# Optimization experiments

Hardware: AMD Instinct MI355X
Metric: run time of the kernel (lower is better)

## Reference

```python
import jax, jax.numpy as jnp
import numpy as np

N = 4096        # nodes
E = 65536       # edges (avg degree 16)
L = 64          # latent_dims
K = 256         # kernel_dims
ED = 6          # edge_dims
DEPTH = 2


def _gelu(x):
    # torch.nn.GELU / F.gelu default = exact erf form
    return jax.nn.gelu(x, approximate=False)


def setup_inputs() -> dict:
    key = jax.random.key(0)
    ks = jax.random.split(key, 12)
    u = lambda k, shape, fan: jax.random.uniform(k, shape, jnp.float32, -1.0, 1.0) / np.sqrt(fan)
    return {
        "nodes": jax.random.normal(ks[0], (N, L), jnp.float32),
        "edge_index": jax.random.randint(ks[1], (2, E), 0, N, jnp.int32),
        "edge_attr": jax.random.uniform(ks[2], (E, ED), jnp.float32),
        # DenseNet kernel MLP: ED -> K -> K -> L*L (GELU between layers)
        "W1": u(ks[3], (ED, K), ED), "b1": jnp.zeros((K,), jnp.float32),
        "W2": u(ks[4], (K, K), K),  "b2": jnp.zeros((K,), jnp.float32),
        "W3": u(ks[5], (K, L * L), K), "b3": jnp.zeros((L * L,), jnp.float32),
        # NNConv root linear (no bias) + conv bias
        "W_root": u(ks[6], (L, L), L),
        "bias": jnp.zeros((L,), jnp.float32),
    }


def reference(nodes, edge_index, edge_attr, W1, b1, W2, b2, W3, b3, W_root, bias):
    src, dst = edge_index[0], edge_index[1]
    # Edge-conditioned dynamic weights (depend only on edge_attr -> compute once)
    h = _gelu(edge_attr @ W1 + b1)          # [E, K]
    h = _gelu(h @ W2 + b2)                  # [E, K]
    W_edge = (h @ W3 + b3).reshape(E, L, L) # [E, L_in, L_out]

    def conv(x):
        msg = jnp.einsum('ei,eio->eo', x[src], W_edge)          # gather + per-edge matmul
        agg = jax.ops.segment_sum(msg, dst, num_segments=N)     # scatter-add to dst
        return agg + x @ W_root + bias

    x = nodes
    for idx in range(DEPTH):
        x = conv(x)
        if idx < DEPTH - 1:
            x = _gelu(x)
    return x
```

## Files before the change

### kernel.cpp

```cpp
#include <hip/hip_runtime.h>
#include <math.h>

#define NN 4096
#define NE 65536
#define LL 64
#define KK 256
#define ED 6
#define MAXSUPER 6144

typedef __bf16 bf16_t;
typedef __attribute__((ext_vector_type(4))) __bf16 bf16x4;
typedef __attribute__((ext_vector_type(8))) __bf16 bf16x8;
typedef __attribute__((ext_vector_type(4))) float f32x4;
typedef __attribute__((ext_vector_type(16))) float f32x16;

#define OFF_CNT    ((size_t)0)
#define OFF_DESC   ((size_t)16384)
#define OFF_AGG0   ((size_t)147456)
#define OFF_AGG1   ((size_t)1196032)
#define ZERO_BYTES ((size_t)2244608)
#define OFF_CURSOR ((size_t)2244608)
#define OFF_SORTED ((size_t)2260992)
#define OFF_W2R    ((size_t)2785280)
#define OFF_W3RR   ((size_t)2916352)
#define OFF_Q0     ((size_t)5013504)
#define OFF_Q1     ((size_t)6062080)
#define OFF_X1F    ((size_t)7110656)
#define OFF_X0BF   ((size_t)8159232)
#define OFF_X1BF   ((size_t)8683520)
#define OFF_H      ((size_t)9207808)
#define OFF_P      ((size_t)42762240)

__device__ __forceinline__ float gelu_f(float x) {
    return 0.5f * x * (1.0f + erff(x * 0.7071067811865476f));
}
__device__ __forceinline__ bf16_t f2bf(float x) { return (bf16_t)x; }

__global__ void k_hist(const int* __restrict__ ei, int* __restrict__ cnt) {
    int e = blockIdx.x * 256 + threadIdx.x;
    atomicAdd(&cnt[ei[e]], 1);
}

__global__ void k_scan(const int* __restrict__ cnt, int* __restrict__ cursor,
                       int4* __restrict__ descs) {
    __shared__ int pd[1024], pc[1024];
    int t = threadIdx.x;
    int deg[4]; int sd = 0, sc = 0;
#pragma unroll
    for (int j = 0; j < 4; j++) {
        deg[j] = cnt[t * 4 + j];
        sd += deg[j];
        sc += (deg[j] + 31) >> 5;
    }
    pd[t] = sd; pc[t] = sc;
    __syncthreads();
    for (int off = 1; off < 1024; off <<= 1) {
        int vd = 0, vc = 0;
        if (t >= off) { vd = pd[t - off]; vc = pc[t - off]; }
        __syncthreads();
        pd[t] += vd; pc[t] += vc;
        __syncthreads();
    }
    int rd = (t > 0) ? pd[t - 1] : 0;
    int rc = (t > 0) ? pc[t - 1] : 0;
    for (int j = 0; j < 4; j++) {
        int v = t * 4 + j, d = deg[j];
        cursor[v] = rd;
        int nch = (d + 31) >> 5;
        for (int c = 0; c < nch; c++) {
            int rem = d - c * 32;
            descs[rc + c] = make_int4(v, rd + c * 32, rem < 32 ? rem : 32, 0);
        }
        rc += nch; rd += d;
    }
}

__global__ void __launch_bounds__(256) k_fuse3(
        const int* __restrict__ ei, int* __restrict__ cursor, int2* __restrict__ sorted,
        const float* __restrict__ W3, bf16_t* __restrict__ W3rr,
        const float* __restrict__ W2, bf16_t* __restrict__ W2r,
        const float* __restrict__ attr, const float* __restrict__ W1,
        const float* __restrict__ b1, bf16_t* __restrict__ a1,
        const float* __restrict__ x, const float* __restrict__ b3,
        bf16_t* __restrict__ xbf, float* __restrict__ Q) {
    __shared__ float smem[4096];
    int bid = blockIdx.x, tid = threadIdx.x;
    if (bid < 256) {
        int e = bid * 256 + tid;
        int s = ei[e], d = ei[NE + e];
        int pos = atomicAdd(&cursor[s], 1);
        sorted[pos] = make_int2(e, d);
    } else if (bid < 512) {
        int k0 = bid - 256;
        for (int idx = tid; idx < 4096; idx += 256)
            smem[idx] = W3[(size_t)k0 * 4096 + idx];
        __syncthreads();
        int sbase = (2 * (k0 >> 4)) * 512 + (((k0 >> 3) & 1) * 32) * 8 + (k0 & 7);
#pragma unroll
        for (int m = 0; m < 2; m++) {
            int w = m * 256 + tid;
            int o = w >> 3, ib = w & 7;
            int s = sbase + (o >> 5) * 512 + (o & 31) * 8;
            int f = (s >> 4) * 1024 + (ib >> 2) * 512 + (ib & 3) * 128 + (s & 15) * 8;
            bf16x8 pk;
#pragma unroll
            for (int j = 0; j < 8; j++) pk[j] = f2bf(smem[(ib * 8 + j) * 64 + o]);
            *(bf16x8*)(W3rr + f) = pk;
        }
    } else if (bid < 768) {
        int t = (bid - 512) * 256 + tid;
        int kk = t >> 13, nn = (t >> 9) & 15, lane = (t >> 3) & 63, j = t & 7;
        int k = kk * 32 + (lane >> 4) * 8 + j;
        int n = nn * 16 + (lane & 15);
        W2r[t] = f2bf(W2[k * 256 + n]);
    } else if (bid < 1792) {
        float* sa = smem;
        int e0 = (bid - 768) * 64;
        for (int i = tid; i < 64 * ED; i += 256) sa[i] = attr[(size_t)e0 * ED + i];
        int col4 = (tid & 63) * 4;
        float w[ED][4], bb[4];
#pragma unroll
        for (int j = 0; j < ED; j++)
#pragma unroll
            for (int c = 0; c < 4; c++) w[j][c] = W1[j * 256 + col4 + c];
#pragma unroll
        for (int c = 0; c < 4; c++) bb[c] = b1[col4 + c];
        __syncthreads();
        int esub = tid >> 6;
#pragma unroll 1
        for (int eg = 0; eg < 16; eg++) {
            int el = eg * 4 + esub;
            float av[ED];
#pragma unroll
            for (int j = 0; j < ED; j++) av[j] = sa[el * ED + j];
            bf16x4 ov;
#pragma unroll
            for (int c = 0; c < 4; c++) {
                float acc = bb[c];
#pragma unroll
                for (int j = 0; j < ED; j++) acc += av[j] * w[j][c];
                ov[c] = f2bf(gelu_f(acc));
            }
            *(bf16x4*)(a1 + (size_t)(e0 + el) * 256 + col4) = ov;
        }
    } else {
        int v = (bid - 1792) * 4 + (tid >> 6);
        int o = tid & 63;
        float xv = x[v * 64 + o];
        smem[tid] = xv;
        xbf[v * 64 + o] = f2bf(xv);
        __syncthreads();
        const float* sx = smem + (tid >> 6) * 64;
        float q = 0.0f;
#pragma unroll 8
        for (int i = 0; i < 64; i++) q += sx[i] * b3[i * 64 + o];
        Q[v * 64 + o] = q;
    }
}

__device__ __forceinline__ void pgemm_body(const bf16_t* __restrict__ xbf,
                                           const bf16_t* __restrict__ W3rr,
                                           bf16_t* __restrict__ P,
                                           bf16_t* __restrict__ sw_wave,
                                           int strip, int rg) {
    int wave = threadIdx.x >> 6, lane = threadIdx.x & 63;
    int col = lane & 15, quad = lane >> 4;
    int half = lane >> 5, l5 = lane & 31;
    bf16_t* sw = sw_wave + wave * 4224;
    bf16x8 b[16][2];
#pragma unroll
    for (int nn = 0; nn < 16; nn++) {
        int sn = strip * 16 + nn;
#pragma unroll
        for (int ki = 0; ki < 2; ki++)
            b[nn][ki] = *(const bf16x8*)(W3rr + (size_t)(sn * 2 + ki) * 512 + lane * 8);
    }
#pragma unroll 1
    for (int rt = 0; rt < 4; rt++) {
        int rowbase = rg * 256 + wave * 64 + rt * 16;
        const bf16_t* arow = xbf + (size_t)(rowbase + col) * 64;
        bf16x8 a0 = *(const bf16x8*)(arow + quad * 8);
        bf16x8 a1v = *(const bf16x8*)(arow + 32 + quad * 8);
#pragma unroll
        for (int nn = 0; nn < 16; nn++) {
            f32x4 acc;
#pragma unroll
            for (int r = 0; r < 4; r++) acc[r] = 0.0f;
            acc = __builtin_amdgcn_mfma_f32_16x16x32_bf16(b[nn][0], a0, acc, 0, 0, 0);
            acc = __builtin_amdgcn_mfma_f32_16x16x32_bf16(b[nn][1], a1v, acc, 0, 0, 0);
            bf16x4 pk;
#pragma unroll
            for (int r = 0; r < 4; r++) pk[r] = f2bf(acc[r]);
            *(bf16x4*)(sw + col * 264 + nn * 16 + quad * 4) = pk;
        }
        __builtin_amdgcn_wave_barrier();
#pragma unroll
        for (int i = 0; i < 8; i++) {
            int r2 = 2 * i + half;
            int vrow = rowbase + r2;
            bf16x8 vb = *(const bf16x8*)(sw + r2 * 264 + l5 * 8);
            int cphys = ((strip >> 1) + vrow * 5) & 31;
            *(bf16x8*)(P + (size_t)vrow * 16384 + cphys * 512 +
                       (strip & 1) * 256 + l5 * 8) = vb;
        }
        __builtin_amdgcn_wave_barrier();
    }
}

__global__ void __launch_bounds__(256) k_fuse4(const bf16_t* __restrict__ xbf,
                                               const bf16_t* __restrict__ W3rr,
                                               bf16_t* __restrict__ P,
                                               const bf16_t* __restrict__ a1,
                                               const bf16_t* __restrict__ W2r,
                                               const float* __restrict__ b2,
                                               bf16_t* __restrict__ h) {
    __shared__ bf16_t sB[16896];
    if (blockIdx.x < 1024) {
        pgemm_body(xbf, W3rr, P, sB, blockIdx.x & 63, blockIdx.x >> 6);
    } else {
        int tid = threadIdx.x;
        int wave = tid >> 6, lane = tid & 63, col = lane & 15, quad = lane >> 4;
        int base = (blockIdx.x - 1024) * 128 + wave * 32;
        bf16x8 a[2][8];
#pragma unroll
        for (int t = 0; t < 2; t++) {
            const bf16_t* arow = a1 + (size_t)(base + t * 16 + col) * 256;
#pragma unroll
            for (int kk = 0; kk < 8; kk++)
                a[t][kk] = *(const bf16x8*)(arow + kk * 32 + quad * 8);
        }
#pragma unroll 1
        for (int p = 0; p < 4; p++) {
#pragma unroll
            for (int it = 0; it < 8; it++) {
                int c = it * 256 + tid;
                int fl = c >> 6;
                int e = (c & 63) * 8;
                int kk = fl >> 2, nnl = fl & 3;
                *(bf16x8*)(sB + fl * 512 + e) =
                    *(const bf16x8*)(W2r + (size_t)(kk * 16 + p * 4 + nnl) * 512 + e);
            }
            __syncthreads();
#pragma unroll
            for (int nnl = 0; nnl < 4; nnl++) {
                f32x4 acc0, acc1;
#pragma unroll
                for (int r = 0; r < 4; r++) { acc0[r] = 0.0f; acc1[r] = 0.0f; }
#pragma unroll
                for (int kk = 0; kk < 8; kk++) {
                    bf16x8 b = *(const bf16x8*)(sB + (kk * 4 + nnl) * 512 + lane * 8);
                    acc0 = __builtin_amdgcn_mfma_f32_16x16x32_bf16(a[0][kk], b, acc0, 0, 0, 0);
                    acc1 = __builtin_amdgcn_mfma_f32_16x16x32_bf16(a[1][kk], b, acc1, 0, 0, 0);
                }
                int ncol = (p * 4 + nnl) * 16 + col;
                float bv = b2[ncol];
#pragma unroll
                for (int r = 0; r < 4; r++) {
                    int row0 = base + quad * 4 + r;
                    h[(size_t)row0 * 256 + ncol] = f2bf(gelu_f(acc0[r] + bv));
                    h[(size_t)(row0 + 16) * 256 + ncol] = f2bf(gelu_f(acc1[r] + bv));
                }
            }
            __syncthreads();
        }
    }
}

__global__ void __launch_bounds__(256) k_pgemm(const bf16_t* __restrict__ xbf,
                                               const bf16_t* __restrict__ W3rr,
                                               bf16_t* __restrict__ P) {
    __shared__ bf16_t sw_all[16896];
    pgemm_body(xbf, W3rr, P, sw_all, blockIdx.x & 63, blockIdx.x >> 6);
}

__global__ void __launch_bounds__(256) k_agg(const int4* __restrict__ descs,
                                             const int2* __restrict__ sorted,
                                             const bf16_t* __restrict__ h,
                                             const bf16_t* __restrict__ P,
                                             const float* __restrict__ Q,
                                             float* __restrict__ agg) {
    int chunk = blockIdx.x * 4 + (threadIdx.x >> 6);
    int lane = threadIdx.x & 63;
    int row = lane & 31, khalf = lane >> 5;
    int4 d = descs[chunk];
    int v = d.x, base = d.y, cnt = d.z;
    if (cnt == 0) return;
    bool valid = (row < cnt);
    int2 ed = sorted[base + (valid ? row : 0)];
    int eid = ed.x, dst = ed.y;

    bf16x8 zero;
#pragma unroll
    for (int i = 0; i < 8; i++) zero[i] = (bf16_t)0.0f;

    bf16x8 a[16];
    const bf16_t* hrow = h + (size_t)eid * 256;
#pragma unroll
    for (int kt = 0; kt < 16; kt++) {
        bf16x8 t = *(const bf16x8*)(hrow + kt * 16 + khalf * 8);
        a[kt] = valid ? t : zero;
    }
    const bf16_t* Pv = P + (size_t)v * 16384;
    int rot = v * 5;
    f32x16 acc0, acc1;
#pragma unroll
    for (int r = 0; r < 16; r++) { acc0[r] = 0.0f; acc1[r] = 0.0f; }
#pragma unroll
    for (int kt = 0; kt < 16; kt++) {
        int c0 = (kt * 2 + 0 + rot) & 31;
        int c1 = (kt * 2 + 1 + rot) & 31;
        bf16x8 b0 = *(const bf16x8*)(Pv + c0 * 512 + lane * 8);
        bf16x8 b1 = *(const bf16x8*)(Pv + c1 * 512 + lane * 8);
        acc0 = __builtin_amdgcn_mfma_f32_32x32x16_bf16(a[kt], b0, acc0, 0, 0, 0);
        acc1 = __builtin_amdgcn_mfma_f32_32x32x16_bf16(a[kt], b1, acc1, 0, 0, 0);
    }
    float q0 = Q[v * 64 + row];
    float q1 = Q[v * 64 + 32 + row];
#pragma unroll
    for (int r = 0; r < 16; r++) {
        int mm = (r & 3) + 8 * (r >> 2) + 4 * khalf;
        int de = __shfl(dst, mm, 64);
        if (mm < cnt) {
            atomicAdd(&agg[(size_t)de * 64 + row], acc0[r] + q0);
            atomicAdd(&agg[(size_t)de * 64 + 32 + row], acc1[r] + q1);
        }
    }
}

__global__ void k_combine1(const float* __restrict__ x, const float* __restrict__ agg,
                           const float* __restrict__ Wroot, const float* __restrict__ bias,
                           const float* __restrict__ b3, float* __restrict__ x1,
                           bf16_t* __restrict__ x1bf, float* __restrict__ Q1) {
    __shared__ float sx[64], sy[64];
    int v = blockIdx.x, o = threadIdx.x;
    sx[o] = x[v * 64 + o];
    __syncthreads();
    float acc = agg[v * 64 + o] + bias[o];
#pragma unroll 8
    for (int i = 0; i < 64; i++) acc += sx[i] * Wroot[i * 64 + o];
    acc = gelu_f(acc);
    x1[v * 64 + o] = acc;
    x1bf[v * 64 + o] = f2bf(acc);
    sy[o] = acc;
    __syncthreads();
    float q = 0.0f;
#pragma unroll 8
    for (int i = 0; i < 64; i++) q += sy[i] * b3[i * 64 + o];
    Q1[v * 64 + o] = q;
}

__global__ void k_combine2(const float* __restrict__ x1, const float* __restrict__ agg,
                           const float* __restrict__ Wroot, const float* __restrict__ bias,
                           float* __restrict__ out) {
    __shared__ float sx[64];
    int v = blockIdx.x, o = threadIdx.x;
    sx[o] = x1[v * 64 + o];
    __syncthreads();
    float acc = agg[v * 64 + o] + bias[o];
#pragma unroll 8
    for (int i = 0; i < 64; i++) acc += sx[i] * Wroot[i * 64 + o];
    out[v * 64 + o] = acc;
}

extern "C" void kernel_launch(void* const* d_in, const int* in_sizes, int n_in,
                              void* d_out, int out_size, void* d_ws, size_t ws_size,
                              hipStream_t stream) {
    const float* nodes = (const float*)d_in[0];
    const int*   ei    = (const int*)d_in[1];
    const float* attr  = (const float*)d_in[2];
    const float* W1    = (const float*)d_in[3];
    const float* b1    = (const float*)d_in[4];
    const float* W2    = (const float*)d_in[5];
    const float* b2    = (const float*)d_in[6];
    const float* W3    = (const float*)d_in[7];
    const float* b3    = (const float*)d_in[8];
    const float* Wroot = (const float*)d_in[9];
    const float* bias  = (const float*)d_in[10];
    float* out = (float*)d_out;
    char* ws = (char*)d_ws;

    int*    cnt    = (int*)(ws + OFF_CNT);
    int4*   descs  = (int4*)(ws + OFF_DESC);
    float*  agg0   = (float*)(ws + OFF_AGG0);
    float*  agg1   = (float*)(ws + OFF_AGG1);
    int*    cursor = (int*)(ws + OFF_CURSOR);
    int2*   sorted = (int2*)(ws + OFF_SORTED);
    bf16_t* W2r    = (bf16_t*)(ws + OFF_W2R);
    bf16_t* W3rr   = (bf16_t*)(ws + OFF_W3RR);
    float*  Q0     = (float*)(ws + OFF_Q0);
    float*  Q1     = (float*)(ws + OFF_Q1);
    float*  x1f    = (float*)(ws + OFF_X1F);
    bf16_t* x0bf   = (bf16_t*)(ws + OFF_X0BF);
    bf16_t* x1bf   = (bf16_t*)(ws + OFF_X1BF);
    bf16_t* hbuf   = (bf16_t*)(ws + OFF_H);
    bf16_t* a1buf  = (bf16_t*)(ws + OFF_H);
    bf16_t* Pbuf   = (bf16_t*)(ws + OFF_P);

    hipMemsetAsync(ws, 0, ZERO_BYTES, stream);
    k_hist<<<NE / 256, 256, 0, stream>>>(ei, cnt);
    k_scan<<<1, 1024, 0, stream>>>(cnt, cursor, descs);
    k_fuse3<<<2816, 256, 0, stream>>>(ei, cursor, sorted, W3, W3rr, W2, W2r,
                                      attr, W1, b1, a1buf, nodes, b3, x0bf, Q0);
    k_fuse4<<<1536, 256, 0, stream>>>(x0bf, W3rr, Pbuf, a1buf, W2r, b2, hbuf);
    k_agg<<<MAXSUPER / 4, 256, 0, stream>>>(descs, sorted, hbuf, Pbuf, Q0, agg0);
    k_combine1<<<NN, 64, 0, stream>>>(nodes, agg0, Wroot, bias, b3, x1f, x1bf, Q1);
    k_pgemm<<<1024, 256, 0, stream>>>(x1bf, W3rr, Pbuf);
    k_agg<<<MAXSUPER / 4, 256, 0, stream>>>(descs, sorted, hbuf, Pbuf, Q1, agg1);
    k_combine2<<<NN, 64, 0, stream>>>(x1f, agg1, Wroot, bias, out);
}
```

Measured before the change: 259.9 us.

## Store first-layer activations in source-sorted order to make edge gathers contiguous

The counting-sort scatter moves into the first-layer MLP blocks, so each edge's a1 row is written at its sorted position. The hidden activations h then come out in sorted order, and the aggregation kernel reads them contiguously by position instead of gathering through edge ids. The sorted array shrinks to destination indices only. The cost is scattered bf16x4 writes of a1 and atomics inside the MLP blocks. The restrict qualifiers on a1 and h are dropped because they alias the same buffer.

```diff
diff --git a/kernel.cpp b/kernel.cpp
--- a/kernel.cpp
+++ b/kernel.cpp
@@ -20,7 +20,7 @@
 #define OFF_AGG1   ((size_t)1196032)
 #define ZERO_BYTES ((size_t)2244608)
 #define OFF_CURSOR ((size_t)2244608)
-#define OFF_SORTED ((size_t)2260992)
+#define OFF_DSTS   ((size_t)2260992)
 #define OFF_W2R    ((size_t)2785280)
 #define OFF_W3RR   ((size_t)2916352)
 #define OFF_Q0     ((size_t)5013504)
@@ -76,7 +76,7 @@
 }
 
 __global__ void __launch_bounds__(256) k_fuse3(
-        const int* __restrict__ ei, int* __restrict__ cursor, int2* __restrict__ sorted,
+        const int* __restrict__ ei, int* __restrict__ cursor, int* __restrict__ dsts,
         const float* __restrict__ W3, bf16_t* __restrict__ W3rr,
         const float* __restrict__ W2, bf16_t* __restrict__ W2r,
         const float* __restrict__ attr, const float* __restrict__ W1,
@@ -86,12 +86,7 @@
     __shared__ float smem[4096];
     int bid = blockIdx.x, tid = threadIdx.x;
     if (bid < 256) {
-        int e = bid * 256 + tid;
-        int s = ei[e], d = ei[NE + e];
-        int pos = atomicAdd(&cursor[s], 1);
-        sorted[pos] = make_int2(e, d);
-    } else if (bid < 512) {
-        int k0 = bid - 256;
+        int k0 = bid;
         for (int idx = tid; idx < 4096; idx += 256)
             smem[idx] = W3[(size_t)k0 * 4096 + idx];
         __syncthreads();
@@ -107,16 +102,24 @@
             for (int j = 0; j < 8; j++) pk[j] = f2bf(smem[(ib * 8 + j) * 64 + o]);
             *(bf16x8*)(W3rr + f) = pk;
         }
-    } else if (bid < 768) {
-        int t = (bid - 512) * 256 + tid;
+    } else if (bid < 512) {
+        int t = (bid - 256) * 256 + tid;
         int kk = t >> 13, nn = (t >> 9) & 15, lane = (t >> 3) & 63, j = t & 7;
         int k = kk * 32 + (lane >> 4) * 8 + j;
         int n = nn * 16 + (lane & 15);
         W2r[t] = f2bf(W2[k * 256 + n]);
-    } else if (bid < 1792) {
+    } else if (bid < 1536) {
         float* sa = smem;
-        int e0 = (bid - 768) * 64;
+        int* spos = (int*)(smem + 512);
+        int e0 = (bid - 512) * 64;
         for (int i = tid; i < 64 * ED; i += 256) sa[i] = attr[(size_t)e0 * ED + i];
+        if (tid < 64) {
+            int e = e0 + tid;
+            int s = ei[e], d = ei[NE + e];
+            int p = atomicAdd(&cursor[s], 1);
+            dsts[p] = d;
+            spos[tid] = p;
+        }
         int col4 = (tid & 63) * 4;
         float w[ED][4], bb[4];
 #pragma unroll
@@ -130,6 +133,7 @@
 #pragma unroll 1
         for (int eg = 0; eg < 16; eg++) {
             int el = eg * 4 + esub;
+            int pos = spos[el];
             float av[ED];
 #pragma unroll
             for (int j = 0; j < ED; j++) av[j] = sa[el * ED + j];
@@ -141,10 +145,10 @@
                 for (int j = 0; j < ED; j++) acc += av[j] * w[j][c];
                 ov[c] = f2bf(gelu_f(acc));
             }
-            *(bf16x4*)(a1 + (size_t)(e0 + el) * 256 + col4) = ov;
+            *(bf16x4*)(a1 + (size_t)pos * 256 + col4) = ov;
         }
     } else {
-        int v = (bid - 1792) * 4 + (tid >> 6);
+        int v = (bid - 1536) * 4 + (tid >> 6);
         int o = tid & 63;
         float xv = x[v * 64 + o];
         smem[tid] = xv;
@@ -210,10 +214,10 @@
 __global__ void __launch_bounds__(256) k_fuse4(const bf16_t* __restrict__ xbf,
                                                const bf16_t* __restrict__ W3rr,
                                                bf16_t* __restrict__ P,
-                                               const bf16_t* __restrict__ a1,
+                                               const bf16_t* a1,
                                                const bf16_t* __restrict__ W2r,
                                                const float* __restrict__ b2,
-                                               bf16_t* __restrict__ h) {
+                                               bf16_t* h) {
     __shared__ bf16_t sB[16896];
     if (blockIdx.x < 1024) {
         pgemm_body(xbf, W3rr, P, sB, blockIdx.x & 63, blockIdx.x >> 6);
@@ -274,7 +278,7 @@
 }
 
 __global__ void __launch_bounds__(256) k_agg(const int4* __restrict__ descs,
-                                             const int2* __restrict__ sorted,
+                                             const int* __restrict__ dsts,
                                              const bf16_t* __restrict__ h,
                                              const bf16_t* __restrict__ P,
                                              const float* __restrict__ Q,
@@ -286,15 +290,15 @@
     int v = d.x, base = d.y, cnt = d.z;
     if (cnt == 0) return;
     bool valid = (row < cnt);
-    int2 ed = sorted[base + (valid ? row : 0)];
-    int eid = ed.x, dst = ed.y;
+    int pos = base + (valid ? row : 0);
+    int dst = dsts[pos];
 
     bf16x8 zero;
 #pragma unroll
     for (int i = 0; i < 8; i++) zero[i] = (bf16_t)0.0f;
 
     bf16x8 a[16];
-    const bf16_t* hrow = h + (size_t)eid * 256;
+    const bf16_t* hrow = h + (size_t)pos * 256;
 #pragma unroll
     for (int kt = 0; kt < 16; kt++) {
         bf16x8 t = *(const bf16x8*)(hrow + kt * 16 + khalf * 8);
@@ -384,7 +388,7 @@
     float*  agg0   = (float*)(ws + OFF_AGG0);
     float*  agg1   = (float*)(ws + OFF_AGG1);
     int*    cursor = (int*)(ws + OFF_CURSOR);
-    int2*   sorted = (int2*)(ws + OFF_SORTED);
+    int*    dsts   = (int*)(ws + OFF_DSTS);
     bf16_t* W2r    = (bf16_t*)(ws + OFF_W2R);
     bf16_t* W3rr   = (bf16_t*)(ws + OFF_W3RR);
     float*  Q0     = (float*)(ws + OFF_Q0);
@@ -399,12 +403,12 @@
     hipMemsetAsync(ws, 0, ZERO_BYTES, stream);
     k_hist<<<NE / 256, 256, 0, stream>>>(ei, cnt);
     k_scan<<<1, 1024, 0, stream>>>(cnt, cursor, descs);
-    k_fuse3<<<2816, 256, 0, stream>>>(ei, cursor, sorted, W3, W3rr, W2, W2r,
+    k_fuse3<<<2560, 256, 0, stream>>>(ei, cursor, dsts, W3, W3rr, W2, W2r,
                                       attr, W1, b1, a1buf, nodes, b3, x0bf, Q0);
     k_fuse4<<<1536, 256, 0, stream>>>(x0bf, W3rr, Pbuf, a1buf, W2r, b2, hbuf);
-    k_agg<<<MAXSUPER / 4, 256, 0, stream>>>(descs, sorted, hbuf, Pbuf, Q0, agg0);
+    k_agg<<<MAXSUPER / 4, 256, 0, stream>>>(descs, dsts, hbuf, Pbuf, Q0, agg0);
     k_combine1<<<NN, 64, 0, stream>>>(nodes, agg0, Wroot, bias, b3, x1f, x1bf, Q1);
     k_pgemm<<<1024, 256, 0, stream>>>(x1bf, W3rr, Pbuf);
-    k_agg<<<MAXSUPER / 4, 256, 0, stream>>>(descs, sorted, hbuf, Pbuf, Q1, agg1);
+    k_agg<<<MAXSUPER / 4, 256, 0, stream>>>(descs, dsts, hbuf, Pbuf, Q1, agg1);
     k_combine2<<<NN, 64, 0, stream>>>(x1f, agg1, Wroot, bias, out);
 }
```

After: 260.9 us. Within noise of the previous version (+0.4%).
